# Kernel optimization log

Measured on AMD Instinct MI355X. Metric: run time of the kernel, lower is better.

Reference implementation:

```python
import jax, jax.numpy as jnp
import numpy as np

N = 1_500_000
NUM_VOXELS = 262_144  # static segment count (replaces torch.unique's dynamic voxel count)
VSIZE = np.array([0.32, 0.32, 0.32], np.float32)
PC_MIN = np.array([-74.88, -74.88, -2.0], np.float32)
GRID = np.array([468, 468, 32], np.int64)
BN_EPS = 1e-3


def setup_inputs() -> dict:
    rng = np.random.default_rng(0)
    # points uniformly inside the point-cloud range -> the range mask is all-true
    xyz = rng.uniform(PC_MIN, PC_MIN + VSIZE * GRID - 1e-3, size=(N, 3)).astype(np.float32)
    feats = rng.uniform(0.0, 1.0, size=(N, 1)).astype(np.float32)
    coords = np.floor((xyz - PC_MIN) / VSIZE).astype(np.int64)
    merge = coords[:, 0] * (GRID[1] * GRID[2]) + coords[:, 1] * GRID[2] + coords[:, 2]
    unq_inv = (merge % NUM_VOXELS).astype(np.int32)  # static-size stand-in for unique inverse ids
    key = jax.random.key(0)
    k1, k2 = jax.random.split(key)
    return {
        'points_xyz': jnp.asarray(xyz),
        'point_feats': jnp.asarray(feats),
        'w1': jax.random.normal(k1, (11, 32), jnp.float32) * 0.1,
        'g1': jnp.ones((32,), jnp.float32),
        'b1': jnp.zeros((32,), jnp.float32),
        'w2': jax.random.normal(k2, (64, 64), jnp.float32) * 0.1,
        'g2': jnp.ones((64,), jnp.float32),
        'b2': jnp.zeros((64,), jnp.float32),
        'unq_inv': jnp.asarray(unq_inv),
    }


def _pfn(x, w, g, b, unq_inv):
    # Linear(bias=False) -> BatchNorm1d(train-mode batch stats, eps=1e-3) -> ReLU -> scatter_max
    y = x @ w
    mu = jnp.mean(y, axis=0)
    var = jnp.var(y, axis=0)
    y = (y - mu) * jax.lax.rsqrt(var + BN_EPS) * g + b
    y = jax.nn.relu(y)
    # relu output >= 0; clamp empty segments (-inf) to 0, matching torch_scatter's zero fill
    y_max = jnp.maximum(jax.ops.segment_max(y, unq_inv, num_segments=NUM_VOXELS), 0.0)
    return y, y_max


def reference(points_xyz, point_feats, w1, g1, b1, w2, g2, b2, unq_inv):
    vsize = jnp.asarray(VSIZE)
    pc_min = jnp.asarray(PC_MIN)
    coords = jnp.floor((points_xyz - pc_min) / vsize)  # [N,3] float voxel coords

    # scatter_mean of xyz per voxel -> cluster-relative offsets
    ones = jnp.ones((points_xyz.shape[0],), points_xyz.dtype)
    cnt = jax.ops.segment_sum(ones, unq_inv, num_segments=NUM_VOXELS)
    vsum = jax.ops.segment_sum(points_xyz, unq_inv, num_segments=NUM_VOXELS)
    vmean = vsum / jnp.maximum(cnt, 1.0)[:, None]
    f_cluster = points_xyz - vmean[unq_inv]

    # offset from voxel center
    f_center = points_xyz - (coords * vsize + vsize * 0.5 + pc_min)
    dist = jnp.linalg.norm(points_xyz, axis=1, keepdims=True)

    feat = jnp.concatenate([points_xyz, point_feats, f_cluster, f_center, dist], axis=-1)  # [N,11]

    x, x_max = _pfn(feat, w1, g1, b1, unq_inv)            # [N,32], [V,32]
    x = jnp.concatenate([x, x_max[unq_inv]], axis=1)       # [N,64]
    _, out = _pfn(x, w2, g2, b2, unq_inv)                  # [V,64] pillar features
    return out
```

## Files before the change

### kernel.cpp

```cpp
#include <hip/hip_runtime.h>

#define NPTS 1500000
#define NVOX 262144
#define BN_EPS 1e-3f
#define PAD 1500160
#define NB_PT 5860
#define NB_L2 11720

typedef __attribute__((ext_vector_type(8))) short bf16x8;
typedef __attribute__((ext_vector_type(4))) float f32x4;

__device__ __forceinline__ unsigned fkey(float f) {
    unsigned u = __float_as_uint(f);
    return u ^ ((unsigned)(((int)u) >> 31) | 0x80000000u);
}
__device__ __forceinline__ float funkey(unsigned k) {
    unsigned u = (k & 0x80000000u) ? (k ^ 0x80000000u) : ~k;
    return __uint_as_float(u);
}
#define KEY_NEG_INF 0x007FFFFFu

__device__ __forceinline__ float bf2f(unsigned short h) {
    union { unsigned u; float f; } x; x.u = ((unsigned)h) << 16; return x.f;
}
__device__ __forceinline__ unsigned short f2bf(float f) {
    union { float f; unsigned u; } x; x.f = f;
    unsigned r = x.u + 0x7FFFu + ((x.u >> 16) & 1u);
    return (unsigned short)(r >> 16);
}
__device__ __forceinline__ unsigned packbf(float a, float b) {
    return (unsigned)f2bf(a) | ((unsigned)f2bf(b) << 16);
}

__device__ __forceinline__ void make_feat(float x, float y, float z, float w,
                                          float mx, float my, float mz, float* f) {
    const float VS = 0.32f;
    const float PMX = -74.88f, PMY = -74.88f, PMZ = -2.0f;
    f[0] = x; f[1] = y; f[2] = z; f[3] = w;
    f[4] = x - mx; f[5] = y - my; f[6] = z - mz;
    float cx = floorf((x - PMX) / VS);
    float cy = floorf((y - PMY) / VS);
    float cz = floorf((z - PMZ) / VS);
    f[7] = x - (cx * VS + 0.5f * VS + PMX);
    f[8] = y - (cy * VS + 0.5f * VS + PMY);
    f[9] = z - (cz * VS + 0.5f * VS + PMZ);
    f[10] = sqrtf(x * x + y * y + z * z);
}

__global__ void k_init(unsigned* __restrict__ okeys, unsigned* __restrict__ xmraw,
                       int* __restrict__ cntv, float* __restrict__ zf,
                       int* __restrict__ svid, const float* __restrict__ w2,
                       uint4* __restrict__ wfrag) {
    long t0 = (long)blockIdx.x * 256 + threadIdx.x;
    long st = (long)gridDim.x * 256;
    uint4 kneg = make_uint4(KEY_NEG_INF, KEY_NEG_INF, KEY_NEG_INF, KEY_NEG_INF);
    for (long i = t0; i < (long)NVOX * 16; i += st) ((uint4*)okeys)[i] = kneg;
    for (long i = t0; i < (long)NVOX * 8; i += st) ((uint4*)xmraw)[i] = kneg;
    for (long i = t0; i < NVOX / 4; i += st) ((int4*)cntv)[i] = make_int4(0, 0, 0, 0);
    for (long i = t0; i < (1024 + 256 * 64 + 256 * 128) / 4; i += st)
        ((float4*)zf)[i] = make_float4(0.f, 0.f, 0.f, 0.f);
    if (t0 < PAD - NPTS) svid[NPTS + t0] = -1;
    if (blockIdx.x == 0 && threadIdx.x < 64) {
        int l = threadIdx.x;
        int lr = l & 15, lk = l >> 4;
        #pragma unroll
        for (int nt = 0; nt < 4; ++nt)
            #pragma unroll
            for (int kt = 0; kt < 2; ++kt) {
                int col = nt * 16 + lr;
                int kb = kt * 32 + lk * 8;
                unsigned u[4];
                #pragma unroll
                for (int j = 0; j < 4; ++j) {
                    float a = w2[(kb + 2 * j) * 64 + col];
                    float b = w2[(kb + 2 * j + 1) * 64 + col];
                    u[j] = packbf(a, b);
                }
                wfrag[(nt * 2 + kt) * 64 + l] = make_uint4(u[0], u[1], u[2], u[3]);
            }
    }
}

__global__ void k_hist(const int* __restrict__ unq, int* __restrict__ cntv) {
    int i = blockIdx.x * blockDim.x + threadIdx.x;
    if (i < NPTS) atomicAdd(&cntv[unq[i]], 1);
}

__global__ void k_scanA(const int* __restrict__ cntv, int* __restrict__ startv,
                        int* __restrict__ bsum) {
    __shared__ int lds[256];
    int t = threadIdx.x;
    int idx4 = blockIdx.x * 256 + t;
    int4 cv = ((const int4*)cntv)[idx4];
    int s0 = cv.x, s1 = s0 + cv.y, s2 = s1 + cv.z, T = s2 + cv.w;
    lds[t] = T;
    __syncthreads();
    for (int o = 1; o < 256; o <<= 1) {
        int v = (t >= o) ? lds[t - o] : 0;
        __syncthreads();
        lds[t] += v;
        __syncthreads();
    }
    int excl = lds[t] - T;
    int4 ov; ov.x = excl; ov.y = excl + s0; ov.z = excl + s1; ov.w = excl + s2;
    ((int4*)startv)[idx4] = ov;
    if (t == 255) bsum[blockIdx.x] = lds[255];
}

__global__ void k_scanB(int* __restrict__ bsum) {
    __shared__ int lds[256];
    int t = threadIdx.x;
    int b = bsum[t];
    lds[t] = b;
    __syncthreads();
    for (int o = 1; o < 256; o <<= 1) {
        int v = (t >= o) ? lds[t - o] : 0;
        __syncthreads();
        lds[t] += v;
        __syncthreads();
    }
    bsum[t] = lds[t] - b;
}

__global__ void k_scanC(int* __restrict__ startv, int* __restrict__ offv,
                        const int* __restrict__ bsum) {
    int t = threadIdx.x;
    int idx4 = blockIdx.x * 256 + t;
    int add = bsum[blockIdx.x];
    int4 v = ((int4*)startv)[idx4];
    v.x += add; v.y += add; v.z += add; v.w += add;
    ((int4*)startv)[idx4] = v;
    ((int4*)offv)[idx4] = v;
}

__global__ void k_scatter2(const float* __restrict__ xyz, const float* __restrict__ pf,
                           const int* __restrict__ unq, int* __restrict__ offv,
                           float4* __restrict__ spts, int* __restrict__ svid) {
    int i = blockIdx.x * blockDim.x + threadIdx.x;
    if (i >= NPTS) return;
    int v = unq[i];
    int pos = atomicAdd(&offv[v], 1);
    float4 p;
    p.x = xyz[3 * i + 0]; p.y = xyz[3 * i + 1]; p.z = xyz[3 * i + 2]; p.w = pf[i];
    spts[pos] = p;
    svid[pos] = v;
}

__global__ void k_vmean2(const float4* __restrict__ spts, const int* __restrict__ cntv,
                         const int* __restrict__ startv, float4* __restrict__ vmeanv) {
    int v = blockIdx.x * 256 + threadIdx.x;
    int cnt = cntv[v];
    if (!cnt) return;
    int st = startv[v];
    float sx = 0, sy = 0, sz = 0;
    for (int j = 0; j < cnt; ++j) {
        float4 p = spts[st + j];
        sx += p.x; sy += p.y; sz += p.z;
    }
    float inv = 1.0f / (float)cnt;
    vmeanv[v] = make_float4(sx * inv, sy * inv, sz * inv, 0.f);
}

__device__ __forceinline__ void flush32(int v, float m, bool atom, int c,
                                        unsigned* __restrict__ xm) {
    if ((unsigned)v >= (unsigned)NVOX) return;
    if (atom) atomicMax(&xm[(size_t)v * 32 + c], fkey(m));
    else xm[(size_t)v * 32 + c] = fkey(m);
}
__device__ __forceinline__ void flush64(int v, float m, bool atom, int c,
                                        unsigned* __restrict__ ok) {
    if ((unsigned)v >= (unsigned)NVOX) return;
    if (atom) atomicMax(&ok[(size_t)v * 64 + c], fkey(m));
    else ok[(size_t)v * 64 + c] = fkey(m);
}

__global__ __launch_bounds__(256) void k_passA(
    const float4* __restrict__ spts, const int* __restrict__ svid,
    const float4* __restrict__ vmeanv, const float* __restrict__ w1,
    unsigned* __restrict__ xmraw, unsigned* __restrict__ y1bf,
    float* __restrict__ spart1) {
    __shared__ float ylds[4][32 * 33];
    int t = threadIdx.x;
    int lane = t & 63, wave = t >> 6;
    int rl = lane & 31, half = lane >> 5;
    long grow = (long)blockIdx.x * 128 + wave * 32 + rl;
    int vid = svid[grow];
    float yv[16];
    #pragma unroll
    for (int j = 0; j < 16; ++j) yv[j] = 0.f;
    if (vid >= 0) {
        float4 p = spts[grow];
        float4 vm = vmeanv[vid];
        float f[11];
        make_feat(p.x, p.y, p.z, p.w, vm.x, vm.y, vm.z, f);
        const float4* w1f = (const float4*)w1;
        #pragma unroll
        for (int k = 0; k < 11; ++k) {
            float fk = f[k];
            #pragma unroll
            for (int q = 0; q < 4; ++q) {
                float4 wq = w1f[k * 8 + half * 4 + q];
                yv[4 * q + 0] = fmaf(fk, wq.x, yv[4 * q + 0]);
                yv[4 * q + 1] = fmaf(fk, wq.y, yv[4 * q + 1]);
                yv[4 * q + 2] = fmaf(fk, wq.z, yv[4 * q + 2]);
                yv[4 * q + 3] = fmaf(fk, wq.w, yv[4 * q + 3]);
            }
        }
    }
    {
        unsigned ypk[8];
        #pragma unroll
        for (int q = 0; q < 8; ++q) ypk[q] = packbf(yv[2 * q], yv[2 * q + 1]);
        uint4* yb = (uint4*)y1bf;
        yb[grow * 4 + half * 2 + 0] = *(const uint4*)&ypk[0];
        yb[grow * 4 + half * 2 + 1] = *(const uint4*)&ypk[4];
    }
    float* yw = &ylds[wave][0];
    #pragma unroll
    for (int j = 0; j < 16; ++j) yw[rl * 33 + half * 16 + j] = yv[j];
    asm volatile("s_waitcnt lgkmcnt(0)" ::: "memory");
    __builtin_amdgcn_sched_barrier(0);
    int c = rl;
    float sa = 0.f, sq = 0.f;
    int cur_v = -2; float cur_m = 0.f; bool first = true;
    #pragma unroll
    for (int i = 0; i < 16; ++i) {
        int r = half * 16 + i;
        float y = yw[r * 33 + c];
        int v = __shfl(vid, r);
        sa += y; sq += y * y;
        if (i == 0) { cur_v = v; cur_m = y; }
        else if (v == cur_v) cur_m = fmaxf(cur_m, y);
        else {
            flush32(cur_v, cur_m, first, c, xmraw);
            first = false; cur_v = v; cur_m = y;
        }
    }
    flush32(cur_v, cur_m, true, c, xmraw);
    sa += __shfl_xor(sa, 32);
    sq += __shfl_xor(sq, 32);
    if (half == 0) {
        int slot = (blockIdx.x * 4 + wave) & 255;
        atomicAdd(&spart1[slot * 64 + c], sa);
        atomicAdd(&spart1[slot * 64 + 32 + c], sq);
    }
}

__global__ void k_fin1(const float* __restrict__ spart1, float* __restrict__ stats,
                       const float* __restrict__ g1, const float* __restrict__ b1) {
    __shared__ float cs[64];
    int t = threadIdx.x;
    float s = 0.f;
    for (int r = 0; r < 256; ++r) s += spart1[r * 64 + t];
    cs[t] = s;
    __syncthreads();
    if (t < 32) {
        float invn = 1.0f / (float)NPTS;
        float mu = cs[t] * invn;
        float var = cs[32 + t] * invn - mu * mu;
        float sc = rsqrtf(var + BN_EPS) * g1[t];
        stats[64 + t] = sc;
        stats[96 + t] = b1[t] - mu * sc;
    }
}

__global__ __launch_bounds__(256) void k_l2(
    const int* __restrict__ svid, const unsigned* __restrict__ y1bf,
    const unsigned* __restrict__ xmraw, const uint4* __restrict__ wfrag,
    const float* __restrict__ stats, float* __restrict__ spart2,
    unsigned* __restrict__ okeys) {
    __shared__ unsigned shbuf[4][1088];
    int t = threadIdx.x;
    int lane = t & 63, wave = t >> 6;
    int rl = lane & 31, half = lane >> 5;
    int lr = lane & 15, lk = lane >> 4;
    long brow = (long)blockIdx.x * 128 + wave * 32;
    int vid = svid[brow + rl];

    uint4 bw[8];
    #pragma unroll
    for (int q = 0; q < 8; ++q) bw[q] = wfrag[q * 64 + lane];
    uint4 yu0 = ((const uint4*)y1bf)[(brow + rl) * 4 + half * 2];
    uint4 yu1 = ((const uint4*)y1bf)[(brow + rl) * 4 + half * 2 + 1];

    unsigned zpk[8], xpk[8];
    if (vid >= 0) {
        const uint4* xr = (const uint4*)(xmraw + (size_t)vid * 32);
        uint4 xq[4];
        #pragma unroll
        for (int q = 0; q < 4; ++q) xq[q] = xr[half * 4 + q];
        const unsigned* xu = (const unsigned*)xq;
        unsigned yw[8] = {yu0.x, yu0.y, yu0.z, yu0.w, yu1.x, yu1.y, yu1.z, yu1.w};
        #pragma unroll
        for (int q = 0; q < 4; ++q) {
            float4 sc = ((const float4*)(stats + 64))[half * 4 + q];
            float4 sh = ((const float4*)(stats + 96))[half * 4 + q];
            float yA = bf2f((unsigned short)(yw[2 * q] & 0xFFFF));
            float yB = bf2f((unsigned short)(yw[2 * q] >> 16));
            float yC = bf2f((unsigned short)(yw[2 * q + 1] & 0xFFFF));
            float yD = bf2f((unsigned short)(yw[2 * q + 1] >> 16));
            zpk[2 * q + 0] = packbf(fmaxf(0.f, fmaf(yA, sc.x, sh.x)),
                                    fmaxf(0.f, fmaf(yB, sc.y, sh.y)));
            zpk[2 * q + 1] = packbf(fmaxf(0.f, fmaf(yC, sc.z, sh.z)),
                                    fmaxf(0.f, fmaf(yD, sc.w, sh.w)));
            float x0 = fmaxf(0.f, fmaf(funkey(xu[4 * q + 0]), sc.x, sh.x));
            float x1 = fmaxf(0.f, fmaf(funkey(xu[4 * q + 1]), sc.y, sh.y));
            float x2 = fmaxf(0.f, fmaf(funkey(xu[4 * q + 2]), sc.z, sh.z));
            float x3 = fmaxf(0.f, fmaf(funkey(xu[4 * q + 3]), sc.w, sh.w));
            xpk[2 * q + 0] = packbf(x0, x1);
            xpk[2 * q + 1] = packbf(x2, x3);
        }
    } else {
        #pragma unroll
        for (int q = 0; q < 8; ++q) { zpk[q] = 0u; xpk[q] = 0u; }
    }
    {
        uint4* arow = (uint4*)&shbuf[wave][rl * 32];
        int sw = rl & 7;
        arow[(2 * half + 0) ^ sw] = *(const uint4*)&zpk[0];
        arow[(2 * half + 1) ^ sw] = *(const uint4*)&zpk[4];
        arow[(4 + 2 * half) ^ sw] = *(const uint4*)&xpk[0];
        arow[(5 + 2 * half) ^ sw] = *(const uint4*)&xpk[4];
    }
    asm volatile("s_waitcnt lgkmcnt(0)" ::: "memory");
    __builtin_amdgcn_sched_barrier(0);

    bf16x8 afr[2][2];
    #pragma unroll
    for (int mt = 0; mt < 2; ++mt)
        #pragma unroll
        for (int kt = 0; kt < 2; ++kt) {
            int riw = mt * 16 + lr;
            uint4 uu = ((const uint4*)&shbuf[wave][riw * 32])[(kt * 4 + lk) ^ (riw & 7)];
            afr[mt][kt] = __builtin_bit_cast(bf16x8, uu);
        }
    asm volatile("s_waitcnt lgkmcnt(0)" ::: "memory");
    __builtin_amdgcn_sched_barrier(0);

    f32x4 acc[2][4];
    #pragma unroll
    for (int mt = 0; mt < 2; ++mt)
        #pragma unroll
        for (int nt = 0; nt < 4; ++nt) {
            acc[mt][nt] = (f32x4){0.f, 0.f, 0.f, 0.f};
            #pragma unroll
            for (int kt = 0; kt < 2; ++kt)
                acc[mt][nt] = __builtin_amdgcn_mfma_f32_16x16x32_bf16(
                    afr[mt][kt], __builtin_bit_cast(bf16x8, bw[nt * 2 + kt]),
                    acc[mt][nt], 0, 0, 0);
        }

    unsigned* y2w = &shbuf[wave][0];
    #pragma unroll
    for (int mt = 0; mt < 2; ++mt)
        #pragma unroll
        for (int nt = 0; nt < 4; ++nt) {
            int col = nt * 16 + lr;
            int w0 = mt * 8 + lk * 2;
            y2w[col * 17 + w0] = packbf(acc[mt][nt][0], acc[mt][nt][1]);
            y2w[col * 17 + w0 + 1] = packbf(acc[mt][nt][2], acc[mt][nt][3]);
        }

    {
        float sa[4] = {0.f, 0.f, 0.f, 0.f}, sq[4] = {0.f, 0.f, 0.f, 0.f};
        #pragma unroll
        for (int mt = 0; mt < 2; ++mt)
            #pragma unroll
            for (int nt = 0; nt < 4; ++nt)
                #pragma unroll
                for (int e = 0; e < 4; ++e) {
                    float v = acc[mt][nt][e];
                    sa[nt] += v; sq[nt] += v * v;
                }
        #pragma unroll
        for (int nt = 0; nt < 4; ++nt) {
            sa[nt] += __shfl_xor(sa[nt], 16); sa[nt] += __shfl_xor(sa[nt], 32);
            sq[nt] += __shfl_xor(sq[nt], 16); sq[nt] += __shfl_xor(sq[nt], 32);
        }
        if (lk == 0) {
            int slot = (blockIdx.x * 4 + wave) & 255;
            #pragma unroll
            for (int nt = 0; nt < 4; ++nt) {
                atomicAdd(&spart2[slot * 128 + nt * 16 + lr], sa[nt]);
                atomicAdd(&spart2[slot * 128 + 64 + nt * 16 + lr], sq[nt]);
            }
        }
    }
    asm volatile("s_waitcnt lgkmcnt(0)" ::: "memory");
    __builtin_amdgcn_sched_barrier(0);

    {
        int c = lane;
        int cur_v = -2; float cur_m = 0.f; bool first = true;
        #pragma unroll
        for (int q = 0; q < 16; ++q) {
            unsigned u = y2w[c * 17 + q];
            #pragma unroll
            for (int e = 0; e < 2; ++e) {
                float d = bf2f((unsigned short)(e ? (u >> 16) : (u & 0xFFFF)));
                int v = __shfl(vid, 2 * q + e);
                if (q == 0 && e == 0) { cur_v = v; cur_m = d; }
                else if (v == cur_v) cur_m = fmaxf(cur_m, d);
                else {
                    flush64(cur_v, cur_m, first, c, okeys);
                    first = false; cur_v = v; cur_m = d;
                }
            }
        }
        flush64(cur_v, cur_m, true, c, okeys);
    }
}

__global__ void k_fin2(const float* __restrict__ spart2, float* __restrict__ stats,
                       const float* __restrict__ g2, const float* __restrict__ b2) {
    __shared__ float cs[128];
    int t = threadIdx.x;
    float s = 0.f;
    for (int r = 0; r < 256; ++r) s += spart2[r * 128 + t];
    cs[t] = s;
    __syncthreads();
    if (t < 64) {
        float invn = 1.0f / (float)NPTS;
        float mu = cs[t] * invn;
        float var = cs[64 + t] * invn - mu * mu;
        float sc = rsqrtf(var + BN_EPS) * g2[t];
        stats[256 + t] = sc;
        stats[320 + t] = b2[t] - mu * sc;
    }
}

__global__ void k_out(unsigned* __restrict__ okeys, const float* __restrict__ stats) {
    int i4 = blockIdx.x * 256 + threadIdx.x;
    uint4 u = ((const uint4*)okeys)[i4];
    int c0 = (i4 & 15) * 4;
    float4 o;
    o.x = fmaxf(0.f, fmaf(funkey(u.x), stats[256 + c0 + 0], stats[320 + c0 + 0]));
    o.y = fmaxf(0.f, fmaf(funkey(u.y), stats[256 + c0 + 1], stats[320 + c0 + 1]));
    o.z = fmaxf(0.f, fmaf(funkey(u.z), stats[256 + c0 + 2], stats[320 + c0 + 2]));
    o.w = fmaxf(0.f, fmaf(funkey(u.w), stats[256 + c0 + 3], stats[320 + c0 + 3]));
    ((float4*)okeys)[i4] = o;
}

extern "C" void kernel_launch(void* const* d_in, const int* in_sizes, int n_in,
                              void* d_out, int out_size, void* d_ws, size_t ws_size,
                              hipStream_t stream) {
    const float* xyz = (const float*)d_in[0];
    const float* pf  = (const float*)d_in[1];
    const float* w1  = (const float*)d_in[2];
    const float* g1  = (const float*)d_in[3];
    const float* b1  = (const float*)d_in[4];
    const float* w2  = (const float*)d_in[5];
    const float* g2  = (const float*)d_in[6];
    const float* b2  = (const float*)d_in[7];
    const int*   unq = (const int*)d_in[8];

    float4* spts     = (float4*)d_ws;
    float4* vmeanv   = spts + PAD;
    int* svid        = (int*)(vmeanv + NVOX);
    unsigned* xmraw  = (unsigned*)(svid + PAD);
    int* cntv        = (int*)(xmraw + (size_t)NVOX * 32);
    int* startv      = cntv + NVOX;
    int* offv        = startv + NVOX;
    int* bsum        = offv + NVOX;
    float* stats     = (float*)(bsum + 256);
    float* spart1    = stats + 1024;
    float* spart2    = spart1 + 256 * 64;
    uint4* wfrag     = (uint4*)(spart2 + 256 * 128);
    unsigned* y1bf   = (unsigned*)(wfrag + 512);

    unsigned* okeys = (unsigned*)d_out;

    k_init<<<2048, 256, 0, stream>>>(okeys, xmraw, cntv, stats, svid, w2, wfrag);
    k_hist<<<NB_PT, 256, 0, stream>>>(unq, cntv);
    k_scanA<<<256, 256, 0, stream>>>(cntv, startv, bsum);
    k_scanB<<<1, 256, 0, stream>>>(bsum);
    k_scanC<<<256, 256, 0, stream>>>(startv, offv, bsum);
    k_scatter2<<<NB_PT, 256, 0, stream>>>(xyz, pf, unq, offv, spts, svid);
    k_vmean2<<<NVOX / 256, 256, 0, stream>>>(spts, cntv, startv, vmeanv);
    k_passA<<<NB_L2, 256, 0, stream>>>(spts, svid, vmeanv, w1, xmraw, y1bf, spart1);
    k_fin1<<<1, 64, 0, stream>>>(spart1, stats, g1, b1);
    k_l2<<<NB_L2, 256, 0, stream>>>(svid, y1bf, xmraw, wfrag, stats, spart2, okeys);
    k_fin2<<<1, 128, 0, stream>>>(spart2, stats, g2, b2);
    k_out<<<NVOX * 16 / 256, 256, 0, stream>>>(okeys, stats);
}
```

Baseline: 391.7 us.

## Precompute per-voxel BN-ReLU of layer-1 max, fuse scan kernels, ballot segment boundaries

A new per-voxel kernel applies the layer-1 BN scale/shift, ReLU and bf16 packing to the scattered max once per voxel. It writes the result into the reused spts buffer, so k_l2 gathers 64 bytes of ready bf16 per point instead of 128 bytes of raw keys that it must convert. The scanB kernel is merged into scanC: each block redoes the 256-entry block-sum scan in LDS, which saves one launch. In k_l2 the layer-2 segment-max loop now uses a precomputed ballot mask of voxel boundaries instead of a shuffle and compare per row. The cost is one extra launch and a pass over the voxel maxima.

Result: faster. 378.1 us (-3.5%).

```diff
diff --git a/kernel.cpp b/kernel.cpp
--- a/kernel.cpp
+++ b/kernel.cpp
@@ -107,7 +107,8 @@
     if (t == 255) bsum[blockIdx.x] = lds[255];
 }
 
-__global__ void k_scanB(int* __restrict__ bsum) {
+__global__ void k_scanC(int* __restrict__ startv, int* __restrict__ offv,
+                        const int* __restrict__ bsum) {
     __shared__ int lds[256];
     int t = threadIdx.x;
     int b = bsum[t];
@@ -119,14 +120,8 @@
         lds[t] += v;
         __syncthreads();
     }
-    bsum[t] = lds[t] - b;
-}
-
-__global__ void k_scanC(int* __restrict__ startv, int* __restrict__ offv,
-                        const int* __restrict__ bsum) {
-    int t = threadIdx.x;
+    int add = (blockIdx.x > 0) ? lds[blockIdx.x - 1] : 0;
     int idx4 = blockIdx.x * 256 + t;
-    int add = bsum[blockIdx.x];
     int4 v = ((int4*)startv)[idx4];
     v.x += add; v.y += add; v.z += add; v.w += add;
     ((int4*)startv)[idx4] = v;
@@ -221,11 +216,12 @@
     asm volatile("s_waitcnt lgkmcnt(0)" ::: "memory");
     __builtin_amdgcn_sched_barrier(0);
     int c = rl;
+    int r0 = half * 16;
     float sa = 0.f, sq = 0.f;
     int cur_v = -2; float cur_m = 0.f; bool first = true;
     #pragma unroll
     for (int i = 0; i < 16; ++i) {
-        int r = half * 16 + i;
+        int r = r0 + i;
         float y = yw[r * 33 + c];
         int v = __shfl(vid, r);
         sa += y; sq += y * y;
@@ -264,9 +260,31 @@
     }
 }
 
+__global__ void k_xmz(const unsigned* __restrict__ xmraw,
+                      const float* __restrict__ stats, unsigned* __restrict__ zxm) {
+    int tid = blockIdx.x * 256 + threadIdx.x;
+    int v = tid >> 2, q = tid & 3;
+    uint4 a = ((const uint4*)xmraw)[v * 8 + q * 2];
+    uint4 b = ((const uint4*)xmraw)[v * 8 + q * 2 + 1];
+    float4 sc0 = ((const float4*)(stats + 64))[q * 2];
+    float4 sh0 = ((const float4*)(stats + 96))[q * 2];
+    float4 sc1 = ((const float4*)(stats + 64))[q * 2 + 1];
+    float4 sh1 = ((const float4*)(stats + 96))[q * 2 + 1];
+    uint4 o;
+    o.x = packbf(fmaxf(0.f, fmaf(funkey(a.x), sc0.x, sh0.x)),
+                 fmaxf(0.f, fmaf(funkey(a.y), sc0.y, sh0.y)));
+    o.y = packbf(fmaxf(0.f, fmaf(funkey(a.z), sc0.z, sh0.z)),
+                 fmaxf(0.f, fmaf(funkey(a.w), sc0.w, sh0.w)));
+    o.z = packbf(fmaxf(0.f, fmaf(funkey(b.x), sc1.x, sh1.x)),
+                 fmaxf(0.f, fmaf(funkey(b.y), sc1.y, sh1.y)));
+    o.w = packbf(fmaxf(0.f, fmaf(funkey(b.z), sc1.z, sh1.z)),
+                 fmaxf(0.f, fmaf(funkey(b.w), sc1.w, sh1.w)));
+    ((uint4*)zxm)[v * 4 + q] = o;
+}
+
 __global__ __launch_bounds__(256) void k_l2(
     const int* __restrict__ svid, const unsigned* __restrict__ y1bf,
-    const unsigned* __restrict__ xmraw, const uint4* __restrict__ wfrag,
+    const unsigned* __restrict__ zxm, const uint4* __restrict__ wfrag,
     const float* __restrict__ stats, float* __restrict__ spart2,
     unsigned* __restrict__ okeys) {
     __shared__ unsigned shbuf[4][1088];
@@ -276,20 +294,22 @@
     int lr = lane & 15, lk = lane >> 4;
     long brow = (long)blockIdx.x * 128 + wave * 32;
     int vid = svid[brow + rl];
+    int vprev = __shfl(vid, (lane + 63) & 63);
+    unsigned mask32 = (unsigned)(__ballot(rl > 0 && vid != vprev) & 0xFFFFFFFFull);
 
     uint4 bw[8];
     #pragma unroll
     for (int q = 0; q < 8; ++q) bw[q] = wfrag[q * 64 + lane];
     uint4 yu0 = ((const uint4*)y1bf)[(brow + rl) * 4 + half * 2];
     uint4 yu1 = ((const uint4*)y1bf)[(brow + rl) * 4 + half * 2 + 1];
-
-    unsigned zpk[8], xpk[8];
+    uint4 xa = make_uint4(0, 0, 0, 0), xb = make_uint4(0, 0, 0, 0);
     if (vid >= 0) {
-        const uint4* xr = (const uint4*)(xmraw + (size_t)vid * 32);
-        uint4 xq[4];
-        #pragma unroll
-        for (int q = 0; q < 4; ++q) xq[q] = xr[half * 4 + q];
-        const unsigned* xu = (const unsigned*)xq;
+        xa = ((const uint4*)zxm)[(size_t)vid * 4 + half * 2];
+        xb = ((const uint4*)zxm)[(size_t)vid * 4 + half * 2 + 1];
+    }
+
+    unsigned zpk[8];
+    if (vid >= 0) {
         unsigned yw[8] = {yu0.x, yu0.y, yu0.z, yu0.w, yu1.x, yu1.y, yu1.z, yu1.w};
         #pragma unroll
         for (int q = 0; q < 4; ++q) {
@@ -303,24 +323,18 @@
                                     fmaxf(0.f, fmaf(yB, sc.y, sh.y)));
             zpk[2 * q + 1] = packbf(fmaxf(0.f, fmaf(yC, sc.z, sh.z)),
                                     fmaxf(0.f, fmaf(yD, sc.w, sh.w)));
-            float x0 = fmaxf(0.f, fmaf(funkey(xu[4 * q + 0]), sc.x, sh.x));
-            float x1 = fmaxf(0.f, fmaf(funkey(xu[4 * q + 1]), sc.y, sh.y));
-            float x2 = fmaxf(0.f, fmaf(funkey(xu[4 * q + 2]), sc.z, sh.z));
-            float x3 = fmaxf(0.f, fmaf(funkey(xu[4 * q + 3]), sc.w, sh.w));
-            xpk[2 * q + 0] = packbf(x0, x1);
-            xpk[2 * q + 1] = packbf(x2, x3);
         }
     } else {
         #pragma unroll
-        for (int q = 0; q < 8; ++q) { zpk[q] = 0u; xpk[q] = 0u; }
+        for (int q = 0; q < 8; ++q) zpk[q] = 0u;
     }
     {
         uint4* arow = (uint4*)&shbuf[wave][rl * 32];
         int sw = rl & 7;
         arow[(2 * half + 0) ^ sw] = *(const uint4*)&zpk[0];
         arow[(2 * half + 1) ^ sw] = *(const uint4*)&zpk[4];
-        arow[(4 + 2 * half) ^ sw] = *(const uint4*)&xpk[0];
-        arow[(5 + 2 * half) ^ sw] = *(const uint4*)&xpk[4];
+        arow[(4 + 2 * half) ^ sw] = xa;
+        arow[(5 + 2 * half) ^ sw] = xb;
     }
     asm volatile("s_waitcnt lgkmcnt(0)" ::: "memory");
     __builtin_amdgcn_sched_barrier(0);
@@ -391,23 +405,24 @@
 
     {
         int c = lane;
-        int cur_v = -2; float cur_m = 0.f; bool first = true;
+        float cur_m = 0.f; bool first = true;
         #pragma unroll
         for (int q = 0; q < 16; ++q) {
             unsigned u = y2w[c * 17 + q];
             #pragma unroll
             for (int e = 0; e < 2; ++e) {
+                int r = 2 * q + e;
                 float d = bf2f((unsigned short)(e ? (u >> 16) : (u & 0xFFFF)));
-                int v = __shfl(vid, 2 * q + e);
-                if (q == 0 && e == 0) { cur_v = v; cur_m = d; }
-                else if (v == cur_v) cur_m = fmaxf(cur_m, d);
-                else {
-                    flush64(cur_v, cur_m, first, c, okeys);
-                    first = false; cur_v = v; cur_m = d;
-                }
+                if (r == 0) cur_m = d;
+                else if ((mask32 >> r) & 1u) {
+                    int v = __shfl(vid, r - 1);
+                    flush64(v, cur_m, first, c, okeys);
+                    first = false; cur_m = d;
+                } else cur_m = fmaxf(cur_m, d);
             }
         }
-        flush64(cur_v, cur_m, true, c, okeys);
+        int vlast = __shfl(vid, 31);
+        flush64(vlast, cur_m, true, c, okeys);
     }
 }
 
@@ -467,19 +482,20 @@
     float* spart2    = spart1 + 256 * 64;
     uint4* wfrag     = (uint4*)(spart2 + 256 * 128);
     unsigned* y1bf   = (unsigned*)(wfrag + 512);
+    unsigned* zxm    = (unsigned*)spts;
 
     unsigned* okeys = (unsigned*)d_out;
 
     k_init<<<2048, 256, 0, stream>>>(okeys, xmraw, cntv, stats, svid, w2, wfrag);
     k_hist<<<NB_PT, 256, 0, stream>>>(unq, cntv);
     k_scanA<<<256, 256, 0, stream>>>(cntv, startv, bsum);
-    k_scanB<<<1, 256, 0, stream>>>(bsum);
     k_scanC<<<256, 256, 0, stream>>>(startv, offv, bsum);
     k_scatter2<<<NB_PT, 256, 0, stream>>>(xyz, pf, unq, offv, spts, svid);
     k_vmean2<<<NVOX / 256, 256, 0, stream>>>(spts, cntv, startv, vmeanv);
     k_passA<<<NB_L2, 256, 0, stream>>>(spts, svid, vmeanv, w1, xmraw, y1bf, spart1);
     k_fin1<<<1, 64, 0, stream>>>(spart1, stats, g1, b1);
-    k_l2<<<NB_L2, 256, 0, stream>>>(svid, y1bf, xmraw, wfrag, stats, spart2, okeys);
+    k_xmz<<<NVOX * 4 / 256, 256, 0, stream>>>(xmraw, stats, zxm);
+    k_l2<<<NB_L2, 256, 0, stream>>>(svid, y1bf, zxm, wfrag, stats, spart2, okeys);
     k_fin2<<<1, 128, 0, stream>>>(spart2, stats, g2, b2);
     k_out<<<NVOX * 16 / 256, 256, 0, stream>>>(okeys, stats);
 }
```
